# Kernel tuning notes

Hardware: AMD Instinct MI355X
Metric: run time of the kernel (lower is better)

The kernel has to match this reference:

```python
import jax, jax.numpy as jnp
import numpy as np
import math

D_MODEL = 1024
N_HEADS = 16
Q_PROJ = D_MODEL // 4
KV_PROJ = D_MODEL // 4
DH = D_MODEL // N_HEADS
LN_EPS = 1e-5


def _layernorm(x, gamma, beta):
    mu = jnp.mean(x, axis=-1, keepdims=True)
    var = jnp.mean(jnp.square(x - mu), axis=-1, keepdims=True)
    return (x - mu) * jax.lax.rsqrt(var + LN_EPS) * gamma + beta


def setup_inputs() -> dict:
    key = jax.random.key(0)
    ks = jax.random.split(key, 7)
    B, S = 2, 2048
    x = jax.random.normal(ks[0], (B, S, D_MODEL), dtype=jnp.float32)
    W_dq = 0.01 * jax.random.normal(ks[1], (D_MODEL, Q_PROJ), dtype=jnp.float32)
    W_uq = 0.01 * jax.random.normal(ks[2], (Q_PROJ, D_MODEL), dtype=jnp.float32)
    W_dkv = 0.01 * jax.random.normal(ks[3], (D_MODEL, KV_PROJ), dtype=jnp.float32)
    W_ukv = 0.01 * jax.random.normal(ks[4], (KV_PROJ, 2 * D_MODEL), dtype=jnp.float32)
    W_o = 0.01 * jax.random.normal(ks[5], (D_MODEL, D_MODEL), dtype=jnp.float32)
    return {
        "x": x,
        "W_dq": W_dq, "W_uq": W_uq,
        "q_ln_g": jnp.ones((Q_PROJ,), jnp.float32), "q_ln_b": jnp.zeros((Q_PROJ,), jnp.float32),
        "W_dkv": W_dkv, "W_ukv": W_ukv,
        "kv_ln_g": jnp.ones((KV_PROJ,), jnp.float32), "kv_ln_b": jnp.zeros((KV_PROJ,), jnp.float32),
        "W_o": W_o,
    }


def reference(x, W_dq, W_uq, q_ln_g, q_ln_b, W_dkv, W_ukv, kv_ln_g, kv_ln_b, W_o):
    B, S, D = x.shape
    # low-rank Q path
    cq = _layernorm(x @ W_dq, q_ln_g, q_ln_b)          # [B,S,q_proj]
    Q = cq @ W_uq                                       # [B,S,D]
    # low-rank KV path
    ckv = _layernorm(x @ W_dkv, kv_ln_g, kv_ln_b)       # [B,S,kv_proj]
    KV = ckv @ W_ukv                                    # [B,S,2D]
    K, V = KV[..., :D], KV[..., D:]
    q = Q.reshape(B, S, N_HEADS, DH)
    k = K.reshape(B, S, N_HEADS, DH)
    v = V.reshape(B, S, N_HEADS, DH)
    scores = jnp.einsum("bqhd,bkhd->bhqk", q, k) / math.sqrt(float(DH))
    # faithful to original: multiply by tril mask, then set exact zeros to -inf
    mask = jnp.tril(jnp.ones((S, S), dtype=scores.dtype))
    scores = scores * mask
    scores = jnp.where(scores == 0, -jnp.inf, scores)
    attn = jax.nn.softmax(scores, axis=-1)
    out = jnp.einsum("bhqk,bkhd->bqhd", attn, v).reshape(B, S, D)
    return out @ W_o.T
```

## Files before the change

### kernel.cpp

```cpp
#include <hip/hip_runtime.h>

typedef __bf16 bf16;
typedef __bf16 bf16x4 __attribute__((ext_vector_type(4)));
typedef __bf16 bf16x8 __attribute__((ext_vector_type(8)));
typedef float f32x4 __attribute__((ext_vector_type(4)));

#define D_MODEL 1024
#define PROJ    256
#define SEQ     2048
#define BATCH   2
#define TOK     4096
#define NH      16
#define DH      64
#define NEG_BIG (-1e30f)
#define QSCALE  0.18033688011112042f

#if __has_builtin(__builtin_amdgcn_exp2f)
#define EXP2(x) __builtin_amdgcn_exp2f(x)
#else
#define EXP2(x) exp2f(x)
#endif

typedef __attribute__((address_space(3))) unsigned int  lds_u32;
typedef __attribute__((address_space(1))) unsigned int  glb_u32;

__device__ __forceinline__ void gl2lds16(const void* gsrc, void* ldst) {
    __builtin_amdgcn_global_load_lds((const glb_u32*)gsrc, (lds_u32*)ldst, 16, 0, 0);
}

template <int CTRL>
__device__ __forceinline__ float dppmov(float x) {
    int i = __builtin_bit_cast(int, x);
    i = __builtin_amdgcn_update_dpp(i, i, CTRL, 0xf, 0xf, false);
    return __builtin_bit_cast(float, i);
}
__device__ __forceinline__ float rowsum16(float v) {
    v += dppmov<0xB1>(v);
    v += dppmov<0x4E>(v);
    v += dppmov<0x141>(v);
    v += dppmov<0x140>(v);
    return v;
}

__global__ void prep_weights_kernel(
    const float* __restrict__ W_o,  const float* __restrict__ W_dq,
    const float* __restrict__ W_dkv, const float* __restrict__ W_uq,
    const float* __restrict__ W_ukv, const float* __restrict__ x,
    bf16* __restrict__ Wo16, bf16* __restrict__ Wt_dq, bf16* __restrict__ Wt_dkv,
    bf16* __restrict__ Wt_uq, bf16* __restrict__ Wt_ukv, bf16* __restrict__ x16) {
    const int R0 = 1048576;
    const int R1 = R0 + 262144;
    const int R2 = R1 + 262144;
    const int R3 = R2 + 262144;
    const int R4 = R3 + 524288;
    const int R5 = R4 + 4194304;
    for (int i = blockIdx.x * blockDim.x + threadIdx.x; i < R5;
         i += gridDim.x * blockDim.x) {
        if (i < R0) {
            Wo16[i] = (bf16)W_o[i];
        } else if (i < R1) {
            int j = i - R0, n = j >> 10, k = j & 1023;
            Wt_dq[j] = (bf16)W_dq[k * 256 + n];
        } else if (i < R2) {
            int j = i - R1, n = j >> 10, k = j & 1023;
            Wt_dkv[j] = (bf16)W_dkv[k * 256 + n];
        } else if (i < R3) {
            int j = i - R2, n = j >> 8, k = j & 255;
            Wt_uq[j] = (bf16)W_uq[k * 1024 + n];
        } else if (i < R4) {
            int j = i - R3, n = j >> 8, k = j & 255;
            Wt_ukv[j] = (bf16)W_ukv[k * 2048 + n];
        } else {
            int j = i - R4;
            x16[j] = (bf16)x[j];
        }
    }
}

__global__ __launch_bounds__(256) void gemm_ln_kernel(
    const bf16* __restrict__ x16,
    const bf16* __restrict__ Wt_q, const bf16* __restrict__ Wt_kv,
    const float* __restrict__ q_g, const float* __restrict__ q_b,
    const float* __restrict__ kv_g, const float* __restrict__ kv_b,
    bf16* __restrict__ cq, bf16* __restrict__ ckv) {
    __shared__ alignas(16) bf16 xA[32 * 32];
    __shared__ alignas(16) bf16 wB[256 * 32];
    __shared__ float red1[4][16];
    __shared__ float red2[4][16];

    const int K = 1024;
    const bf16* Wt = blockIdx.y ? Wt_kv : Wt_q;
    const float* gamma = blockIdx.y ? kv_g : q_g;
    const float* beta  = blockIdx.y ? kv_b : q_b;
    bf16* out = blockIdx.y ? ckv : cq;

    const int m0 = blockIdx.x * 32;
    const int wv = threadIdx.x >> 6;
    const int lane = threadIdx.x & 63;
    const int g = lane >> 4;
    const int ln16 = lane & 15;
    const int wr = wv >> 1;
    const int wc = wv & 1;

    const int crow = lane >> 2;
    const int ckc = lane & 3;
    const bf16* gx = x16 + (size_t)(m0 + (wv & 1) * 16 + crow) * K + ckc * 8;
    char* lx = (char*)xA + (wv & 1) * 1024;
    const bf16* gw = Wt + (size_t)(64 * wv + crow) * K + ckc * 8;
    char* lw = (char*)wB + wv * 4096;

    f32x4 acc[8] = {};
    for (int k0 = 0; k0 < K; k0 += 32) {
        if (wv < 2) gl2lds16(gx + k0, lx);
#pragma unroll
        for (int i = 0; i < 4; ++i)
            gl2lds16(gw + (size_t)i * 16 * K + k0, lw + i * 1024);
        __syncthreads();

        bf16x8 a = *(const bf16x8*)(xA + (wr * 16 + ln16) * 32 + g * 8);
#pragma unroll
        for (int t = 0; t < 8; ++t) {
            bf16x8 b = *(const bf16x8*)(wB + (wc * 128 + 16 * t + ln16) * 32 + g * 8);
            acc[t] = __builtin_amdgcn_mfma_f32_16x16x32_bf16(a, b, acc[t], 0, 0, 0);
        }
        __syncthreads();
    }

    float s1[4], s2[4];
#pragma unroll
    for (int r = 0; r < 4; ++r) {
        float a = 0.f, b = 0.f;
#pragma unroll
        for (int t = 0; t < 8; ++t) { float v = acc[t][r]; a += v; b += v * v; }
        s1[r] = rowsum16(a); s2[r] = rowsum16(b);
    }
    if (ln16 == 0) {
#pragma unroll
        for (int r = 0; r < 4; ++r) {
            red1[wv][g * 4 + r] = s1[r];
            red2[wv][g * 4 + r] = s2[r];
        }
    }
    __syncthreads();
#pragma unroll
    for (int r = 0; r < 4; ++r) {
        int rl = g * 4 + r;
        float t1 = red1[wr * 2][rl] + red1[wr * 2 + 1][rl];
        float t2 = red2[wr * 2][rl] + red2[wr * 2 + 1][rl];
        float mu = t1 * (1.0f / 256.0f);
        float var = t2 * (1.0f / 256.0f) - mu * mu;
        float rs = rsqrtf(var + 1e-5f);
        int row = m0 + wr * 16 + rl;
#pragma unroll
        for (int t = 0; t < 8; ++t) {
            int col = wc * 128 + 16 * t + ln16;
            float v = (acc[t][r] - mu) * rs * gamma[col] + beta[col];
            out[(size_t)row * PROJ + col] = (bf16)v;
        }
    }
}

template <typename OutT>
__device__ __forceinline__ void gemm_body(
    const bf16* __restrict__ A, const bf16* __restrict__ Bt,
    OutT* __restrict__ C, bf16* __restrict__ C2, int N, int K,
    int bx, int by, int mode, bf16* tA, bf16* tB) {
    const int w = threadIdx.x >> 6;
    const int lane = threadIdx.x & 63;
    const int g = lane >> 4;
    const int ln16 = lane & 15;
    const int wr = w >> 1;
    const int wc = w & 1;

    const int m0 = bx * 64;
    const int n0 = by * 128;

    const int crow = lane >> 2;
    const int ckc = lane & 3;
    const bf16* gA  = A  + (size_t)(m0 + w * 16 + crow) * K + ckc * 8;
    const bf16* gB0 = Bt + (size_t)(n0 + w * 16 + crow) * K + ckc * 8;
    const bf16* gB1 = Bt + (size_t)(n0 + 64 + w * 16 + crow) * K + ckc * 8;
    char* lA  = (char*)tA + w * 1024;
    char* lB0 = (char*)tB + w * 1024;
    char* lB1 = (char*)tB + 4096 + w * 1024;

    f32x4 acc[2][4] = {};
    for (int k0 = 0; k0 < K; k0 += 32) {
        gl2lds16(gA + k0, lA);
        gl2lds16(gB0 + k0, lB0);
        gl2lds16(gB1 + k0, lB1);
        __syncthreads();

        bf16x8 af[2], bf[4];
#pragma unroll
        for (int s = 0; s < 2; ++s)
            af[s] = *(const bf16x8*)(tA + (wr * 32 + s * 16 + ln16) * 32 + g * 8);
#pragma unroll
        for (int t = 0; t < 4; ++t)
            bf[t] = *(const bf16x8*)(tB + (wc * 64 + t * 16 + ln16) * 32 + g * 8);
#pragma unroll
        for (int s = 0; s < 2; ++s)
#pragma unroll
            for (int t = 0; t < 4; ++t)
                acc[s][t] = __builtin_amdgcn_mfma_f32_16x16x32_bf16(
                    af[s], bf[t], acc[s][t], 0, 0, 0);
        __syncthreads();
    }

#pragma unroll
    for (int s = 0; s < 2; ++s)
#pragma unroll
        for (int t = 0; t < 4; ++t) {
            const int col = n0 + wc * 64 + t * 16 + ln16;
            const int tok0 = m0 + wr * 32 + s * 16 + g * 4;
            if (mode == 2 && col >= 1024) {
                int cc = col - 1024;
                int h = cc >> 6, d = cc & 63;
                int b = tok0 >> 11, sq = tok0 & 2047;
                bf16x4 pk;
#pragma unroll
                for (int r = 0; r < 4; ++r) pk[r] = (bf16)acc[s][t][r];
                *(bf16x4*)(C2 + ((size_t)((b * 16 + h) * 64 + d) * SEQ + sq)) = pk;
            } else {
#pragma unroll
                for (int r = 0; r < 4; ++r) {
                    int row = tok0 + r;
                    float v = acc[s][t][r];
                    if (mode == 0) {
                        C[(size_t)row * N + col] = (OutT)v;
                    } else {
                        if (mode == 1) v *= QSCALE;
                        int h = col >> 6, d = col & 63;
                        int b = row >> 11, sq = row & 2047;
                        C[((size_t)((b * 16 + h) * 2048 + sq)) * 64 + d] = (OutT)v;
                    }
                }
            }
        }
}

__global__ __launch_bounds__(256) void gemm_o_kernel(
    const bf16* __restrict__ A, const bf16* __restrict__ Bt,
    float* __restrict__ C, int M, int N, int K) {
    __shared__ alignas(16) bf16 tA[64 * 32];
    __shared__ alignas(16) bf16 tB[128 * 32];
    gemm_body<float>(A, Bt, C, nullptr, N, K, blockIdx.x, blockIdx.y, 0, tA, tB);
}

__global__ __launch_bounds__(256) void gemm_qkv_kernel(
    const bf16* __restrict__ cq, const bf16* __restrict__ Wt_uq,
    const bf16* __restrict__ ckv, const bf16* __restrict__ Wt_ukv,
    bf16* __restrict__ Qh, bf16* __restrict__ Kh, bf16* __restrict__ Vt) {
    __shared__ alignas(16) bf16 tA[64 * 32];
    __shared__ alignas(16) bf16 tB[128 * 32];
    const int i = blockIdx.x;
    if (i < 512) {
        gemm_body<bf16>(cq, Wt_uq, Qh, nullptr, D_MODEL, PROJ,
                        i >> 3, i & 7, 1, tA, tB);
    } else {
        const int j = i - 512;
        gemm_body<bf16>(ckv, Wt_ukv, Kh, Vt, 2 * D_MODEL, PROJ,
                        j >> 4, j & 15, 2, tA, tB);
    }
}

__device__ __forceinline__ void qk_exp_pack(
    int k0, int q, bool masked, int g, int ln16,
    bf16x8 aq0, bf16x8 aq1, const bf16x8* Kf,
    bf16x8& P1, bf16x8& P2) {
    f32x4 sc[4];
    __builtin_amdgcn_s_setprio(1);
#pragma unroll
    for (int c = 0; c < 4; ++c) {
        f32x4 z = {};
        z = __builtin_amdgcn_mfma_f32_16x16x32_bf16(Kf[2 * c], aq0, z, 0, 0, 0);
        z = __builtin_amdgcn_mfma_f32_16x16x32_bf16(Kf[2 * c + 1], aq1, z, 0, 0, 0);
        sc[c] = z;
    }
    __builtin_amdgcn_s_setprio(0);
    if (masked) {
        const int kb = k0 + 8 * g;
#pragma unroll
        for (int c = 0; c < 4; ++c)
#pragma unroll
            for (int r = 0; r < 4; ++r) {
                int kcol = kb + (c & 1) * 4 + r + ((c >> 1) << 5);
                if (kcol > q) sc[c][r] = NEG_BIG;
            }
    }
#pragma unroll
    for (int c = 0; c < 4; ++c)
#pragma unroll
        for (int r = 0; r < 4; ++r) sc[c][r] = EXP2(sc[c][r]);
#pragma unroll
    for (int r = 0; r < 4; ++r) {
        P1[r] = (bf16)sc[0][r]; P1[4 + r] = (bf16)sc[1][r];
        P2[r] = (bf16)sc[2][r]; P2[4 + r] = (bf16)sc[3][r];
    }
}

__device__ __forceinline__ void pv_accum(
    bf16x8 P1, bf16x8 P2, const bf16x8* Vf, bf16x8 vones,
    f32x4* o, f32x4& oli) {
    __builtin_amdgcn_s_setprio(1);
#pragma unroll
    for (int t = 0; t < 4; ++t) {
        o[t] = __builtin_amdgcn_mfma_f32_16x16x32_bf16(Vf[2 * t], P1, o[t], 0, 0, 0);
        o[t] = __builtin_amdgcn_mfma_f32_16x16x32_bf16(Vf[2 * t + 1], P2, o[t], 0, 0, 0);
    }
    oli = __builtin_amdgcn_mfma_f32_16x16x32_bf16(vones, P1, oli, 0, 0, 0);
    oli = __builtin_amdgcn_mfma_f32_16x16x32_bf16(vones, P2, oli, 0, 0, 0);
    __builtin_amdgcn_s_setprio(0);
}

__global__ __launch_bounds__(256) void attn_kernel(
    const bf16* __restrict__ Qh, const bf16* __restrict__ Kh,
    const bf16* __restrict__ Vt, bf16* __restrict__ AT) {
    __shared__ alignas(128) bf16 kbuf[2][64 * 64];
    __shared__ alignas(128) bf16 vbuf[2][64 * 64];

    const int lane = threadIdx.x & 63;
    const int g = lane >> 4;
    const int ln16 = lane & 15;
    const int wv = threadIdx.x >> 6;

    const int j = blockIdx.x & 255;
    const int rnd = blockIdx.x >> 8;
    const int bh = j & 31;
    const int gg = j >> 5;
    const int super = rnd ? gg : 15 - gg;
    const int nt = 2 * super + 2;
    const int qb = super * 128 + wv * 32;

    const bf16* Kbh = Kh + (size_t)bh * SEQ * DH;
    const bf16* Vbh = Vt + (size_t)bh * DH * SEQ;

    const int rho = lane >> 3;
    const int sl  = lane & 7;
    int kofs[2];
    size_t vofs[2];
#pragma unroll
    for (int i = 0; i < 2; ++i) {
        const int row = 16 * wv + 8 * i + rho;
        const int c = sl ^ ((rho & 3) | ((i & 1) << 2));
        kofs[i] = row * 64 + c * 8;
        vofs[i] = (size_t)row * SEQ + c * 8;
    }

    const int row_base = ((ln16 & 12) << 1) + (ln16 & 3);
    int kro[4], vro[4];
#pragma unroll
    for (int c = 0; c < 4; ++c) {
        const int row = row_base + (c & 1) * 4 + ((c >> 1) << 5);
        const int fr = (row & 3) | (((row >> 3) & 1) << 2);
        kro[c] = row * 128 + (g ^ fr) * 16;
    }
#pragma unroll
    for (int t = 0; t < 4; ++t) {
        const int d = 16 * t + ln16;
        const int fd = (d & 3) | (((d >> 3) & 1) << 2);
        vro[t] = d * 128 + (g ^ fd) * 16;
    }

    bf16x8 aq[2][2];
#pragma unroll
    for (int hh = 0; hh < 2; ++hh) {
        const bf16* qp = Qh + ((size_t)bh * SEQ + qb + 16 * hh + ln16) * DH + g * 8;
        aq[hh][0] = *(const bf16x8*)qp;
        aq[hh][1] = *(const bf16x8*)(qp + 32);
    }

    bf16x8 vones;
#pragma unroll
    for (int i = 0; i < 8; ++i) vones[i] = (bf16)1.0f;

    f32x4 o0[4] = {}, o1[4] = {};
    f32x4 oli0 = {}, oli1 = {};

#pragma unroll
    for (int i = 0; i < 2; ++i) {
        gl2lds16(Kbh + kofs[i], (char*)kbuf + wv * 2048 + i * 1024);
        gl2lds16(Vbh + vofs[i], (char*)vbuf + wv * 2048 + i * 1024);
    }
    __syncthreads();

    int cur = 0;
    for (int kt = 0; kt < nt; ++kt) {
        if (kt + 1 < nt) {
            const size_t k0n = (size_t)(kt + 1) * 64;
            char* kb = (char*)kbuf + (cur ^ 1) * 8192 + wv * 2048;
            char* vb = (char*)vbuf + (cur ^ 1) * 8192 + wv * 2048;
#pragma unroll
            for (int i = 0; i < 2; ++i) {
                gl2lds16(Kbh + k0n * 64 + kofs[i], kb + i * 1024);
                gl2lds16(Vbh + vofs[i] + k0n, vb + i * 1024);
            }
        }

        if (kt * 64 <= qb + 31) {
            const char* kb = (const char*)kbuf + cur * 8192;
            const char* vb = (const char*)vbuf + cur * 8192;
            bf16x8 Kf[8], Vf[8];
#pragma unroll
            for (int c = 0; c < 4; ++c) {
                Kf[2 * c]     = *(const bf16x8*)(kb + kro[c]);
                Kf[2 * c + 1] = *(const bf16x8*)(kb + (kro[c] ^ 64));
            }
#pragma unroll
            for (int t = 0; t < 4; ++t) {
                Vf[2 * t]     = *(const bf16x8*)(vb + vro[t]);
                Vf[2 * t + 1] = *(const bf16x8*)(vb + (vro[t] ^ 64));
            }

            const int k0 = kt * 64;
            const bool msk = (64 * (kt + 1) > qb);
            bf16x8 P1a, P2a, P1b, P2b;
            qk_exp_pack(k0, qb + ln16, msk, g, ln16,
                        aq[0][0], aq[0][1], Kf, P1a, P2a);
            qk_exp_pack(k0, qb + 16 + ln16, msk, g, ln16,
                        aq[1][0], aq[1][1], Kf, P1b, P2b);
            pv_accum(P1a, P2a, Vf, vones, o0, oli0);
            pv_accum(P1b, P2b, Vf, vones, o1, oli1);
        }
        __syncthreads();
        cur ^= 1;
    }

    const float inv0 = 1.0f / oli0[0];
    const float inv1 = 1.0f / oli1[0];
    const int b = bh >> 4, h = bh & 15;
    const size_t tok0 = (size_t)(b * SEQ + qb + ln16) * D_MODEL + h * DH;
    const size_t tok1 = (size_t)(b * SEQ + qb + 16 + ln16) * D_MODEL + h * DH;
#pragma unroll
    for (int t = 0; t < 4; ++t) {
        bf16x4 pk0, pk1;
#pragma unroll
        for (int r = 0; r < 4; ++r) {
            pk0[r] = (bf16)(o0[t][r] * inv0);
            pk1[r] = (bf16)(o1[t][r] * inv1);
        }
        *(bf16x4*)(AT + tok0 + 16 * t + 4 * g) = pk0;
        *(bf16x4*)(AT + tok1 + 16 * t + 4 * g) = pk1;
    }
}

extern "C" void kernel_launch(void* const* d_in, const int* in_sizes, int n_in,
                              void* d_out, int out_size, void* d_ws, size_t ws_size,
                              hipStream_t stream) {
    const float* x     = (const float*)d_in[0];
    const float* W_dq  = (const float*)d_in[1];
    const float* W_uq  = (const float*)d_in[2];
    const float* q_g   = (const float*)d_in[3];
    const float* q_b   = (const float*)d_in[4];
    const float* W_dkv = (const float*)d_in[5];
    const float* W_ukv = (const float*)d_in[6];
    const float* kv_g  = (const float*)d_in[7];
    const float* kv_b  = (const float*)d_in[8];
    const float* W_o   = (const float*)d_in[9];

    char* ws = (char*)d_ws;
    size_t off = 0;
    bf16* Wo16   = (bf16*)(ws + off); off += (size_t)D_MODEL * D_MODEL * 2;
    bf16* Wt_dq  = (bf16*)(ws + off); off += (size_t)PROJ * D_MODEL * 2;
    bf16* Wt_dkv = (bf16*)(ws + off); off += (size_t)PROJ * D_MODEL * 2;
    bf16* Wt_uq  = (bf16*)(ws + off); off += (size_t)D_MODEL * PROJ * 2;
    bf16* Wt_ukv = (bf16*)(ws + off); off += (size_t)(2 * D_MODEL) * PROJ * 2;
    bf16* x16    = (bf16*)(ws + off); off += (size_t)TOK * D_MODEL * 2;
    bf16* cq     = (bf16*)(ws + off); off += (size_t)TOK * PROJ * 2;
    bf16* ckv    = (bf16*)(ws + off); off += (size_t)TOK * PROJ * 2;
    bf16* Qh     = (bf16*)(ws + off); off += (size_t)TOK * D_MODEL * 2;
    bf16* Kh     = (bf16*)(ws + off); off += (size_t)TOK * D_MODEL * 2;
    bf16* Vt     = (bf16*)(ws + off); off += (size_t)TOK * D_MODEL * 2;
    bf16* AT     = (bf16*)(ws + off); off += (size_t)TOK * D_MODEL * 2;

    prep_weights_kernel<<<2048, 256, 0, stream>>>(
        W_o, W_dq, W_dkv, W_uq, W_ukv, x,
        Wo16, Wt_dq, Wt_dkv, Wt_uq, Wt_ukv, x16);

    gemm_ln_kernel<<<dim3(TOK / 32, 2), 256, 0, stream>>>(
        x16, Wt_dq, Wt_dkv, q_g, q_b, kv_g, kv_b, cq, ckv);

    gemm_qkv_kernel<<<1536, 256, 0, stream>>>(cq, Wt_uq, ckv, Wt_ukv, Qh, Kh, Vt);

    attn_kernel<<<512, 256, 0, stream>>>(Qh, Kh, Vt, AT);

    gemm_o_kernel<<<dim3(TOK / 64, D_MODEL / 128), 256, 0, stream>>>(
        AT, Wo16, (float*)d_out, TOK, D_MODEL, D_MODEL);
}
```

Baseline: 203.4 us.

## Double-buffer GEMM LDS tiles, tile-transpose weights, and shrink attention work per block

Splits weight preparation into a plain conversion kernel and an LDS-tiled transpose kernel, so the strided uncoalesced transposed reads go away. The LN-GEMM and shared GEMM body gain double-buffered LDS, prefetching the next K slice before computing on the current one, and the LN-GEMM uses 16-row blocks. The attention kernel now assigns 16 query rows per wave and 64 per block with 1024 blocks, which drops the paired-tile logic and the skip branch. The changes raise LDS use and block count, and the attention split loses K/V reuse across the two query sub-tiles.

```diff
diff --git a/kernel.cpp b/kernel.cpp
--- a/kernel.cpp
+++ b/kernel.cpp
@@ -42,39 +42,45 @@
     return v;
 }
 
-__global__ void prep_weights_kernel(
-    const float* __restrict__ W_o,  const float* __restrict__ W_dq,
-    const float* __restrict__ W_dkv, const float* __restrict__ W_uq,
-    const float* __restrict__ W_ukv, const float* __restrict__ x,
-    bf16* __restrict__ Wo16, bf16* __restrict__ Wt_dq, bf16* __restrict__ Wt_dkv,
-    bf16* __restrict__ Wt_uq, bf16* __restrict__ Wt_ukv, bf16* __restrict__ x16) {
+__global__ __launch_bounds__(256) void prep_weights_kernel(
+    const float* __restrict__ W_o, const float* __restrict__ x,
+    bf16* __restrict__ Wo16, bf16* __restrict__ x16) {
     const int R0 = 1048576;
-    const int R1 = R0 + 262144;
-    const int R2 = R1 + 262144;
-    const int R3 = R2 + 262144;
-    const int R4 = R3 + 524288;
-    const int R5 = R4 + 4194304;
-    for (int i = blockIdx.x * blockDim.x + threadIdx.x; i < R5;
+    const int R1 = R0 + 4194304;
+    for (int i = blockIdx.x * blockDim.x + threadIdx.x; i < R1;
          i += gridDim.x * blockDim.x) {
-        if (i < R0) {
-            Wo16[i] = (bf16)W_o[i];
-        } else if (i < R1) {
-            int j = i - R0, n = j >> 10, k = j & 1023;
-            Wt_dq[j] = (bf16)W_dq[k * 256 + n];
-        } else if (i < R2) {
-            int j = i - R1, n = j >> 10, k = j & 1023;
-            Wt_dkv[j] = (bf16)W_dkv[k * 256 + n];
-        } else if (i < R3) {
-            int j = i - R2, n = j >> 8, k = j & 255;
-            Wt_uq[j] = (bf16)W_uq[k * 1024 + n];
-        } else if (i < R4) {
-            int j = i - R3, n = j >> 8, k = j & 255;
-            Wt_ukv[j] = (bf16)W_ukv[k * 2048 + n];
-        } else {
-            int j = i - R4;
-            x16[j] = (bf16)x[j];
-        }
-    }
+        if (i < R0) Wo16[i] = (bf16)W_o[i];
+        else        x16[i - R0] = (bf16)x[i - R0];
+    }
+}
+
+__global__ __launch_bounds__(256) void transpose_cvt_kernel(
+    const float* __restrict__ W_dq, const float* __restrict__ W_dkv,
+    const float* __restrict__ W_uq, const float* __restrict__ W_ukv,
+    bf16* __restrict__ Wt_dq, bf16* __restrict__ Wt_dkv,
+    bf16* __restrict__ Wt_uq, bf16* __restrict__ Wt_ukv) {
+    __shared__ float tile[64][65];
+    const int m = blockIdx.y;
+    const float* src; bf16* dst; int R, C;
+    if (m == 0)      { src = W_dq;  dst = Wt_dq;  R = 1024; C = 256; }
+    else if (m == 1) { src = W_dkv; dst = Wt_dkv; R = 1024; C = 256; }
+    else if (m == 2) { src = W_uq;  dst = Wt_uq;  R = 256;  C = 1024; }
+    else             { src = W_ukv; dst = Wt_ukv; R = 256;  C = 2048; }
+    const int tilesC = C >> 6;
+    const int ntile = (R >> 6) * tilesC;
+    const int t = blockIdx.x;
+    if (t >= ntile) return;
+    const int r0 = (t / tilesC) << 6;
+    const int c0 = (t % tilesC) << 6;
+    const int tr = threadIdx.x >> 6;
+    const int tc = threadIdx.x & 63;
+#pragma unroll
+    for (int i = 0; i < 16; ++i)
+        tile[tr * 16 + i][tc] = src[(size_t)(r0 + tr * 16 + i) * C + c0 + tc];
+    __syncthreads();
+#pragma unroll
+    for (int i = 0; i < 16; ++i)
+        dst[(size_t)(c0 + tr * 16 + i) * R + r0 + tc] = (bf16)tile[tc][tr * 16 + i];
 }
 
 __global__ __launch_bounds__(256) void gemm_ln_kernel(
@@ -83,8 +89,8 @@
     const float* __restrict__ q_g, const float* __restrict__ q_b,
     const float* __restrict__ kv_g, const float* __restrict__ kv_b,
     bf16* __restrict__ cq, bf16* __restrict__ ckv) {
-    __shared__ alignas(16) bf16 xA[32 * 32];
-    __shared__ alignas(16) bf16 wB[256 * 32];
+    __shared__ alignas(16) bf16 xA[2][16 * 32];
+    __shared__ alignas(16) bf16 wB[2][256 * 32];
     __shared__ float red1[4][16];
     __shared__ float red2[4][16];
 
@@ -94,36 +100,45 @@
     const float* beta  = blockIdx.y ? kv_b : q_b;
     bf16* out = blockIdx.y ? ckv : cq;
 
-    const int m0 = blockIdx.x * 32;
+    const int m0 = blockIdx.x * 16;
     const int wv = threadIdx.x >> 6;
     const int lane = threadIdx.x & 63;
     const int g = lane >> 4;
     const int ln16 = lane & 15;
-    const int wr = wv >> 1;
-    const int wc = wv & 1;
 
     const int crow = lane >> 2;
     const int ckc = lane & 3;
-    const bf16* gx = x16 + (size_t)(m0 + (wv & 1) * 16 + crow) * K + ckc * 8;
-    char* lx = (char*)xA + (wv & 1) * 1024;
+    const bf16* gx = x16 + (size_t)(m0 + crow) * K + ckc * 8;
     const bf16* gw = Wt + (size_t)(64 * wv + crow) * K + ckc * 8;
-    char* lw = (char*)wB + wv * 4096;
-
-    f32x4 acc[8] = {};
+
+    f32x4 acc[4] = {};
+
+    if (wv == 0) gl2lds16(gx, (char*)xA);
+#pragma unroll
+    for (int i = 0; i < 4; ++i)
+        gl2lds16(gw + (size_t)i * 16 * K, (char*)wB + wv * 4096 + i * 1024);
+    __syncthreads();
+
+    int buf = 0;
     for (int k0 = 0; k0 < K; k0 += 32) {
-        if (wv < 2) gl2lds16(gx + k0, lx);
-#pragma unroll
-        for (int i = 0; i < 4; ++i)
-            gl2lds16(gw + (size_t)i * 16 * K + k0, lw + i * 1024);
+        if (k0 + 32 < K) {
+            const int nb = buf ^ 1;
+            if (wv == 0) gl2lds16(gx + k0 + 32, (char*)xA + nb * 1024);
+#pragma unroll
+            for (int i = 0; i < 4; ++i)
+                gl2lds16(gw + (size_t)i * 16 * K + k0 + 32,
+                         (char*)wB + nb * 16384 + wv * 4096 + i * 1024);
+        }
+        const bf16* cx = &xA[buf][0];
+        const bf16* cw = &wB[buf][0];
+        bf16x8 a = *(const bf16x8*)(cx + ln16 * 32 + g * 8);
+#pragma unroll
+        for (int t = 0; t < 4; ++t) {
+            bf16x8 b = *(const bf16x8*)(cw + (wv * 64 + 16 * t + ln16) * 32 + g * 8);
+            acc[t] = __builtin_amdgcn_mfma_f32_16x16x32_bf16(a, b, acc[t], 0, 0, 0);
+        }
         __syncthreads();
-
-        bf16x8 a = *(const bf16x8*)(xA + (wr * 16 + ln16) * 32 + g * 8);
-#pragma unroll
-        for (int t = 0; t < 8; ++t) {
-            bf16x8 b = *(const bf16x8*)(wB + (wc * 128 + 16 * t + ln16) * 32 + g * 8);
-            acc[t] = __builtin_amdgcn_mfma_f32_16x16x32_bf16(a, b, acc[t], 0, 0, 0);
-        }
-        __syncthreads();
+        buf ^= 1;
     }
 
     float s1[4], s2[4];
@@ -131,7 +146,7 @@
     for (int r = 0; r < 4; ++r) {
         float a = 0.f, b = 0.f;
 #pragma unroll
-        for (int t = 0; t < 8; ++t) { float v = acc[t][r]; a += v; b += v * v; }
+        for (int t = 0; t < 4; ++t) { float v = acc[t][r]; a += v; b += v * v; }
         s1[r] = rowsum16(a); s2[r] = rowsum16(b);
     }
     if (ln16 == 0) {
@@ -145,15 +160,15 @@
 #pragma unroll
     for (int r = 0; r < 4; ++r) {
         int rl = g * 4 + r;
-        float t1 = red1[wr * 2][rl] + red1[wr * 2 + 1][rl];
-        float t2 = red2[wr * 2][rl] + red2[wr * 2 + 1][rl];
+        float t1 = red1[0][rl] + red1[1][rl] + red1[2][rl] + red1[3][rl];
+        float t2 = red2[0][rl] + red2[1][rl] + red2[2][rl] + red2[3][rl];
         float mu = t1 * (1.0f / 256.0f);
         float var = t2 * (1.0f / 256.0f) - mu * mu;
         float rs = rsqrtf(var + 1e-5f);
-        int row = m0 + wr * 16 + rl;
-#pragma unroll
-        for (int t = 0; t < 8; ++t) {
-            int col = wc * 128 + 16 * t + ln16;
+        int row = m0 + rl;
+#pragma unroll
+        for (int t = 0; t < 4; ++t) {
+            int col = wv * 64 + 16 * t + ln16;
             float v = (acc[t][r] - mu) * rs * gamma[col] + beta[col];
             out[(size_t)row * PROJ + col] = (bf16)v;
         }
@@ -180,31 +195,40 @@
     const bf16* gA  = A  + (size_t)(m0 + w * 16 + crow) * K + ckc * 8;
     const bf16* gB0 = Bt + (size_t)(n0 + w * 16 + crow) * K + ckc * 8;
     const bf16* gB1 = Bt + (size_t)(n0 + 64 + w * 16 + crow) * K + ckc * 8;
-    char* lA  = (char*)tA + w * 1024;
-    char* lB0 = (char*)tB + w * 1024;
-    char* lB1 = (char*)tB + 4096 + w * 1024;
 
     f32x4 acc[2][4] = {};
+
+    gl2lds16(gA, (char*)tA + w * 1024);
+    gl2lds16(gB0, (char*)tB + w * 1024);
+    gl2lds16(gB1, (char*)tB + 4096 + w * 1024);
+    __syncthreads();
+
+    int buf = 0;
     for (int k0 = 0; k0 < K; k0 += 32) {
-        gl2lds16(gA + k0, lA);
-        gl2lds16(gB0 + k0, lB0);
-        gl2lds16(gB1 + k0, lB1);
-        __syncthreads();
-
-        bf16x8 af[2], bf[4];
+        if (k0 + 32 < K) {
+            const int nb = buf ^ 1;
+            gl2lds16(gA + k0 + 32, (char*)tA + nb * 4096 + w * 1024);
+            gl2lds16(gB0 + k0 + 32, (char*)tB + nb * 8192 + w * 1024);
+            gl2lds16(gB1 + k0 + 32, (char*)tB + nb * 8192 + 4096 + w * 1024);
+        }
+        const bf16* cA = tA + buf * 2048;
+        const bf16* cB = tB + buf * 4096;
+
+        bf16x8 af[2], bfr[4];
 #pragma unroll
         for (int s = 0; s < 2; ++s)
-            af[s] = *(const bf16x8*)(tA + (wr * 32 + s * 16 + ln16) * 32 + g * 8);
+            af[s] = *(const bf16x8*)(cA + (wr * 32 + s * 16 + ln16) * 32 + g * 8);
 #pragma unroll
         for (int t = 0; t < 4; ++t)
-            bf[t] = *(const bf16x8*)(tB + (wc * 64 + t * 16 + ln16) * 32 + g * 8);
+            bfr[t] = *(const bf16x8*)(cB + (wc * 64 + t * 16 + ln16) * 32 + g * 8);
 #pragma unroll
         for (int s = 0; s < 2; ++s)
 #pragma unroll
             for (int t = 0; t < 4; ++t)
                 acc[s][t] = __builtin_amdgcn_mfma_f32_16x16x32_bf16(
-                    af[s], bf[t], acc[s][t], 0, 0, 0);
+                    af[s], bfr[t], acc[s][t], 0, 0, 0);
         __syncthreads();
+        buf ^= 1;
     }
 
 #pragma unroll
@@ -242,25 +266,26 @@
 __global__ __launch_bounds__(256) void gemm_o_kernel(
     const bf16* __restrict__ A, const bf16* __restrict__ Bt,
     float* __restrict__ C, int M, int N, int K) {
-    __shared__ alignas(16) bf16 tA[64 * 32];
-    __shared__ alignas(16) bf16 tB[128 * 32];
-    gemm_body<float>(A, Bt, C, nullptr, N, K, blockIdx.x, blockIdx.y, 0, tA, tB);
+    __shared__ alignas(16) bf16 tA[2][64 * 32];
+    __shared__ alignas(16) bf16 tB[2][128 * 32];
+    gemm_body<float>(A, Bt, C, nullptr, N, K, blockIdx.x, blockIdx.y, 0,
+                     &tA[0][0], &tB[0][0]);
 }
 
 __global__ __launch_bounds__(256) void gemm_qkv_kernel(
     const bf16* __restrict__ cq, const bf16* __restrict__ Wt_uq,
     const bf16* __restrict__ ckv, const bf16* __restrict__ Wt_ukv,
     bf16* __restrict__ Qh, bf16* __restrict__ Kh, bf16* __restrict__ Vt) {
-    __shared__ alignas(16) bf16 tA[64 * 32];
-    __shared__ alignas(16) bf16 tB[128 * 32];
+    __shared__ alignas(16) bf16 tA[2][64 * 32];
+    __shared__ alignas(16) bf16 tB[2][128 * 32];
     const int i = blockIdx.x;
     if (i < 512) {
         gemm_body<bf16>(cq, Wt_uq, Qh, nullptr, D_MODEL, PROJ,
-                        i >> 3, i & 7, 1, tA, tB);
+                        i >> 3, i & 7, 1, &tA[0][0], &tB[0][0]);
     } else {
         const int j = i - 512;
         gemm_body<bf16>(ckv, Wt_ukv, Kh, Vt, 2 * D_MODEL, PROJ,
-                        j >> 4, j & 15, 2, tA, tB);
+                        j >> 4, j & 15, 2, &tA[0][0], &tB[0][0]);
     }
 }
 
@@ -324,13 +349,11 @@
     const int ln16 = lane & 15;
     const int wv = threadIdx.x >> 6;
 
-    const int j = blockIdx.x & 255;
-    const int rnd = blockIdx.x >> 8;
-    const int bh = j & 31;
-    const int gg = j >> 5;
-    const int super = rnd ? gg : 15 - gg;
-    const int nt = 2 * super + 2;
-    const int qb = super * 128 + wv * 32;
+    const int bh = blockIdx.x & 31;
+    const int qsuper = 31 - (blockIdx.x >> 5);
+    const int nt = qsuper + 1;
+    const int qb = qsuper * 64 + wv * 16;
+    const int q = qb + ln16;
 
     const bf16* Kbh = Kh + (size_t)bh * SEQ * DH;
     const bf16* Vbh = Vt + (size_t)bh * DH * SEQ;
@@ -362,20 +385,15 @@
         vro[t] = d * 128 + (g ^ fd) * 16;
     }
 
-    bf16x8 aq[2][2];
-#pragma unroll
-    for (int hh = 0; hh < 2; ++hh) {
-        const bf16* qp = Qh + ((size_t)bh * SEQ + qb + 16 * hh + ln16) * DH + g * 8;
-        aq[hh][0] = *(const bf16x8*)qp;
-        aq[hh][1] = *(const bf16x8*)(qp + 32);
-    }
+    const bf16* qp = Qh + ((size_t)bh * SEQ + q) * DH + g * 8;
+    bf16x8 aq0 = *(const bf16x8*)qp, aq1 = *(const bf16x8*)(qp + 32);
 
     bf16x8 vones;
 #pragma unroll
     for (int i = 0; i < 8; ++i) vones[i] = (bf16)1.0f;
 
-    f32x4 o0[4] = {}, o1[4] = {};
-    f32x4 oli0 = {}, oli1 = {};
+    f32x4 o[4] = {};
+    f32x4 oli = {};
 
 #pragma unroll
     for (int i = 0; i < 2; ++i) {
@@ -397,50 +415,36 @@
             }
         }
 
-        if (kt * 64 <= qb + 31) {
-            const char* kb = (const char*)kbuf + cur * 8192;
-            const char* vb = (const char*)vbuf + cur * 8192;
-            bf16x8 Kf[8], Vf[8];
-#pragma unroll
-            for (int c = 0; c < 4; ++c) {
-                Kf[2 * c]     = *(const bf16x8*)(kb + kro[c]);
-                Kf[2 * c + 1] = *(const bf16x8*)(kb + (kro[c] ^ 64));
-            }
-#pragma unroll
-            for (int t = 0; t < 4; ++t) {
-                Vf[2 * t]     = *(const bf16x8*)(vb + vro[t]);
-                Vf[2 * t + 1] = *(const bf16x8*)(vb + (vro[t] ^ 64));
-            }
-
-            const int k0 = kt * 64;
-            const bool msk = (64 * (kt + 1) > qb);
-            bf16x8 P1a, P2a, P1b, P2b;
-            qk_exp_pack(k0, qb + ln16, msk, g, ln16,
-                        aq[0][0], aq[0][1], Kf, P1a, P2a);
-            qk_exp_pack(k0, qb + 16 + ln16, msk, g, ln16,
-                        aq[1][0], aq[1][1], Kf, P1b, P2b);
-            pv_accum(P1a, P2a, Vf, vones, o0, oli0);
-            pv_accum(P1b, P2b, Vf, vones, o1, oli1);
-        }
+        const char* kb = (const char*)kbuf + cur * 8192;
+        const char* vb = (const char*)vbuf + cur * 8192;
+        bf16x8 Kf[8], Vf[8];
+#pragma unroll
+        for (int c = 0; c < 4; ++c) {
+            Kf[2 * c]     = *(const bf16x8*)(kb + kro[c]);
+            Kf[2 * c + 1] = *(const bf16x8*)(kb + (kro[c] ^ 64));
+        }
+#pragma unroll
+        for (int t = 0; t < 4; ++t) {
+            Vf[2 * t]     = *(const bf16x8*)(vb + vro[t]);
+            Vf[2 * t + 1] = *(const bf16x8*)(vb + (vro[t] ^ 64));
+        }
+
+        bf16x8 P1, P2;
+        qk_exp_pack(kt * 64, q, kt == qsuper, g, ln16, aq0, aq1, Kf, P1, P2);
+        pv_accum(P1, P2, Vf, vones, o, oli);
         __syncthreads();
         cur ^= 1;
     }
 
-    const float inv0 = 1.0f / oli0[0];
-    const float inv1 = 1.0f / oli1[0];
+    const float inv = 1.0f / oli[0];
     const int b = bh >> 4, h = bh & 15;
-    const size_t tok0 = (size_t)(b * SEQ + qb + ln16) * D_MODEL + h * DH;
-    const size_t tok1 = (size_t)(b * SEQ + qb + 16 + ln16) * D_MODEL + h * DH;
+    const size_t tok = (size_t)(b * SEQ + q) * D_MODEL + h * DH;
 #pragma unroll
     for (int t = 0; t < 4; ++t) {
-        bf16x4 pk0, pk1;
-#pragma unroll
-        for (int r = 0; r < 4; ++r) {
-            pk0[r] = (bf16)(o0[t][r] * inv0);
-            pk1[r] = (bf16)(o1[t][r] * inv1);
-        }
-        *(bf16x4*)(AT + tok0 + 16 * t + 4 * g) = pk0;
-        *(bf16x4*)(AT + tok1 + 16 * t + 4 * g) = pk1;
+        bf16x4 pk;
+#pragma unroll
+        for (int r = 0; r < 4; ++r) pk[r] = (bf16)(o[t][r] * inv);
+        *(bf16x4*)(AT + tok + 16 * t + 4 * g) = pk;
     }
 }
 
@@ -473,16 +477,17 @@
     bf16* Vt     = (bf16*)(ws + off); off += (size_t)TOK * D_MODEL * 2;
     bf16* AT     = (bf16*)(ws + off); off += (size_t)TOK * D_MODEL * 2;
 
-    prep_weights_kernel<<<2048, 256, 0, stream>>>(
-        W_o, W_dq, W_dkv, W_uq, W_ukv, x,
-        Wo16, Wt_dq, Wt_dkv, Wt_uq, Wt_ukv, x16);
-
-    gemm_ln_kernel<<<dim3(TOK / 32, 2), 256, 0, stream>>>(
+    prep_weights_kernel<<<1024, 256, 0, stream>>>(W_o, x, Wo16, x16);
+
+    transpose_cvt_kernel<<<dim3(128, 4), 256, 0, stream>>>(
+        W_dq, W_dkv, W_uq, W_ukv, Wt_dq, Wt_dkv, Wt_uq, Wt_ukv);
+
+    gemm_ln_kernel<<<dim3(TOK / 16, 2), 256, 0, stream>>>(
         x16, Wt_dq, Wt_dkv, q_g, q_b, kv_g, kv_b, cq, ckv);
 
     gemm_qkv_kernel<<<1536, 256, 0, stream>>>(cq, Wt_uq, ckv, Wt_ukv, Qh, Kh, Vt);
 
-    attn_kernel<<<512, 256, 0, stream>>>(Qh, Kh, Vt, AT);
+    attn_kernel<<<1024, 256, 0, stream>>>(Qh, Kh, Vt, AT);
 
     gemm_o_kernel<<<dim3(TOK / 64, D_MODEL / 128), 256, 0, stream>>>(
         AT, Wo16, (float*)d_out, TOK, D_MODEL, D_MODEL);
```

After: 184.3 us. 9.4% less time.
